# Optimization experiments

Hardware: AMD Instinct MI355X
Metric: run time of the kernel (lower is better)

The kernel has to match this reference:

```python
import jax, jax.numpy as jnp
import numpy as np

NUM_HEADS = 4


def _mha_pool(seg):
    """seg: [n_seg, S, H]. First 4 channels are attention logits (softmax over S),
    rest are values split into 4 heads; returns [n_seg, H-4]."""
    n_seg, S, H = seg.shape
    attn = jax.nn.softmax(seg[:, :, :NUM_HEADS], axis=1)          # [n, S, 4]
    vals = seg[:, :, NUM_HEADS:].reshape(n_seg, S, NUM_HEADS, -1)  # [n, S, 4, hd]
    pooled = jnp.einsum('nsh,nshd->nhd', attn, vals)               # [n, 4, hd]
    return pooled.reshape(n_seg, -1)


def setup_inputs() -> dict:
    key = jax.random.key(0)
    k1, k2, k3, k4 = jax.random.split(key, 4)
    T, D, H = 131072, 2048, 260
    embeddings = jax.random.normal(k1, (T, D), dtype=jnp.float32)
    labels = jax.random.randint(k2, (T,), 0, 2, dtype=jnp.int32)
    W_down = jax.random.normal(k3, (D, H), dtype=jnp.float32) / np.sqrt(D)
    b_down = jnp.zeros((H,), dtype=jnp.float32)
    W_final = jax.random.normal(k4, (H - NUM_HEADS, 1), dtype=jnp.float32) / np.sqrt(H - NUM_HEADS)
    b_final = jnp.zeros((1,), dtype=jnp.float32)
    return {
        'embeddings': embeddings,
        'W_down': W_down,
        'b_down': b_down,
        'W_final': W_final,
        'b_final': b_final,
        'labels': labels,
        'tokens_per_problem': 512,
        'tokens_per_line': 16,
    }


def reference(embeddings, W_down, b_down, W_final, b_final, labels,
              tokens_per_problem, tokens_per_line):
    T, D = embeddings.shape
    H = W_down.shape[1]
    # Dropout is identity in eval mode (reference baseline).
    proj = embeddings @ W_down + b_down                      # [T, H]
    # MHA_POOL_4_HEADS: keep attention logits raw, GELU (exact erf) the values.
    act = jnp.concatenate(
        [proj[:, :NUM_HEADS], jax.nn.gelu(proj[:, NUM_HEADS:], approximate=False)],
        axis=1)                                              # [T, H]

    P = T // tokens_per_problem
    problem_feat = _mha_pool(act.reshape(P, tokens_per_problem, H))   # [P, H-4]
    problem_logits = (problem_feat @ W_final + b_final)[:, 0]

    L = T // tokens_per_line
    line_feat = _mha_pool(act.reshape(L, tokens_per_line, H))         # [L, H-4]
    line_logits = (line_feat @ W_final + b_final)[:, 0]

    token_logits = (act[:, NUM_HEADS:] @ W_final + b_final)[:, 0]     # [T]

    problem_labels = labels.reshape(P, tokens_per_problem).min(axis=1)
    line_labels = labels.reshape(L, tokens_per_line).min(axis=1)
    return token_logits, line_logits, line_labels, problem_logits, problem_labels
```

## Files before the change

### kernel.cpp

```cpp
#include <hip/hip_runtime.h>
#include <hip/hip_bf16.h>
#include <math.h>

#define T_TOK   131072
#define D_IN    2048
#define H_CH    260
#define NFRAG_P 18
#define KSTEPS  64
#define STEP_BYTES  (NFRAG_P * 64 * 16)
#define CHUNK_BYTES (2 * STEP_BYTES)
#define NCHUNK  32

typedef __attribute__((ext_vector_type(8))) short bf16x8;
typedef __attribute__((ext_vector_type(4))) float f32x4;

__device__ inline short f2bf(float x) {
    __hip_bfloat16 h = __float2bfloat16(x);
    return __builtin_bit_cast(short, h);
}

__global__ void prep_wfrag(const float* __restrict__ W, __hip_bfloat16* __restrict__ Wf) {
    int g = blockIdx.x;
    int s = g / NFRAG_P, f = g % NFRAG_P;
    int lane = threadIdx.x;
    int k0 = s * 32 + (lane >> 4) * 8;
    int col = f * 16 + (lane & 15);
    short vals8[8];
#pragma unroll
    for (int j = 0; j < 8; j++) {
        float v = (col < H_CH) ? W[(size_t)(k0 + j) * H_CH + col] : 0.f;
        vals8[j] = f2bf(v);
    }
    *reinterpret_cast<bf16x8*>(reinterpret_cast<short*>(Wf) + ((size_t)g * 64 + lane) * 8) =
        *reinterpret_cast<bf16x8*>(vals8);
}

__global__ __launch_bounds__(512, 4)
void gemm_act(const float* __restrict__ emb, const __hip_bfloat16* __restrict__ Wfrag,
              const float* __restrict__ b_down, const float* __restrict__ W_final,
              const float* __restrict__ b_final,
              float* __restrict__ attnL, __hip_bfloat16* __restrict__ vals,
              float* __restrict__ token_logits) {
    __shared__ __align__(16) char smem[2 * CHUNK_BYTES];
    __shared__ float tokred[8][32];

    int wave = threadIdx.x >> 6;
    int lane = threadIdx.x & 63;
    int quad = wave & 3;
    int nhalf = wave >> 2;
    int f0 = nhalf * 9;
    int r0 = blockIdx.x * 128 + quad * 32;
    int row_in = lane & 15;
    int kbase = (lane >> 4) * 8;

    const char* gW = (const char*)Wfrag;

    auto stage_chunk = [&](int c, char* lbase) {
        const char* src = gW + (size_t)c * CHUNK_BYTES;
#pragma unroll
        for (int r = 0; r < 4; ++r) {
            int off = (r * 8 + wave) * 1024;
            __builtin_amdgcn_global_load_lds(
                (const __attribute__((address_space(1))) unsigned int*)(src + off + lane * 16),
                (__attribute__((address_space(3))) unsigned int*)(lbase + off), 16, 0, 0);
        }
        if (wave < 4) {
            int off = (32 + wave) * 1024;
            __builtin_amdgcn_global_load_lds(
                (const __attribute__((address_space(1))) unsigned int*)(src + off + lane * 16),
                (__attribute__((address_space(3))) unsigned int*)(lbase + off), 16, 0, 0);
        }
    };

    f32x4 acc0[9], acc1[9];
#pragma unroll
    for (int f = 0; f < 9; f++) {
        acc0[f] = (f32x4){0.f, 0.f, 0.f, 0.f};
        acc1[f] = (f32x4){0.f, 0.f, 0.f, 0.f};
    }

    const float* ap0 = emb + (size_t)(r0 + row_in) * D_IN + kbase;
    const float* ap1 = ap0 + (size_t)16 * D_IN;

    stage_chunk(0, smem);
    f32x4 c0l = *reinterpret_cast<const f32x4*>(ap0);
    f32x4 c0h = *reinterpret_cast<const f32x4*>(ap0 + 4);
    f32x4 c1l = *reinterpret_cast<const f32x4*>(ap1);
    f32x4 c1h = *reinterpret_cast<const f32x4*>(ap1 + 4);
    f32x4 n0l, n0h, n1l, n1h;
    __syncthreads();

#define DO_STEP(AL0, AH0, AL1, AH1, BOFF)                                         \
    {                                                                             \
        bf16x8 af0, af1;                                                          \
        af0[0] = f2bf(AL0[0]); af0[1] = f2bf(AL0[1]);                             \
        af0[2] = f2bf(AL0[2]); af0[3] = f2bf(AL0[3]);                             \
        af0[4] = f2bf(AH0[0]); af0[5] = f2bf(AH0[1]);                             \
        af0[6] = f2bf(AH0[2]); af0[7] = f2bf(AH0[3]);                             \
        af1[0] = f2bf(AL1[0]); af1[1] = f2bf(AL1[1]);                             \
        af1[2] = f2bf(AL1[2]); af1[3] = f2bf(AL1[3]);                             \
        af1[4] = f2bf(AH1[0]); af1[5] = f2bf(AH1[1]);                             \
        af1[6] = f2bf(AH1[2]); af1[7] = f2bf(AH1[3]);                             \
        const char* bb = smem + (BOFF) + (size_t)f0 * 1024 + lane * 16;           \
        _Pragma("unroll")                                                         \
        for (int f = 0; f < 9; f++) {                                             \
            bf16x8 bfr = *reinterpret_cast<const bf16x8*>(bb + f * 1024);         \
            acc0[f] = __builtin_amdgcn_mfma_f32_16x16x32_bf16(af0, bfr, acc0[f], 0, 0, 0); \
            acc1[f] = __builtin_amdgcn_mfma_f32_16x16x32_bf16(af1, bfr, acc1[f], 0, 0, 0); \
        }                                                                         \
    }

    for (int c = 0; c < NCHUNK; ++c) {
        int base = (c & 1) * CHUNK_BYTES;
        if (c + 1 < NCHUNK) stage_chunk(c + 1, smem + ((c + 1) & 1) * CHUNK_BYTES);

        int off1 = (2 * c + 1) * 32;
        n0l = *reinterpret_cast<const f32x4*>(ap0 + off1);
        n0h = *reinterpret_cast<const f32x4*>(ap0 + off1 + 4);
        n1l = *reinterpret_cast<const f32x4*>(ap1 + off1);
        n1h = *reinterpret_cast<const f32x4*>(ap1 + off1 + 4);
        DO_STEP(c0l, c0h, c1l, c1h, base)

        int s2 = 2 * c + 2;
        int off2 = (s2 < KSTEPS ? s2 : 0) * 32;
        c0l = *reinterpret_cast<const f32x4*>(ap0 + off2);
        c0h = *reinterpret_cast<const f32x4*>(ap0 + off2 + 4);
        c1l = *reinterpret_cast<const f32x4*>(ap1 + off2);
        c1h = *reinterpret_cast<const f32x4*>(ap1 + off2 + 4);
        DO_STEP(n0l, n0h, n1l, n1h, base + STEP_BYTES)

        __syncthreads();
    }
#undef DO_STEP

    int colbase = lane & 15;
    int rgroup = (lane >> 4) * 4;
    float tp0[4] = {0.f, 0.f, 0.f, 0.f};
    float tp1[4] = {0.f, 0.f, 0.f, 0.f};
#pragma unroll
    for (int f = 0; f < 9; f++) {
        int n = (f0 + f) * 16 + colbase;
        float bias = (n < H_CH) ? b_down[n] : 0.f;
        float wf = (n >= 4 && n < H_CH) ? W_final[n - 4] : 0.f;
#pragma unroll
        for (int i = 0; i < 4; i++) {
            int row0 = r0 + rgroup + i;
            int row1 = row0 + 16;
            float v0 = acc0[f][i] + bias;
            float v1 = acc1[f][i] + bias;
            float a0 = (n < 4) ? v0 : 0.5f * v0 * (1.f + erff(v0 * 0.70710678118f));
            float a1 = (n < 4) ? v1 : 0.5f * v1 * (1.f + erff(v1 * 0.70710678118f));
            if (n < 4) {
                attnL[(size_t)row0 * 4 + n] = v0;
                attnL[(size_t)row1 * 4 + n] = v1;
            } else if (n < H_CH) {
                vals[(size_t)row0 * 256 + (n - 4)] = __float2bfloat16(a0);
                vals[(size_t)row1 * 256 + (n - 4)] = __float2bfloat16(a1);
            }
            tp0[i] += a0 * wf;
            tp1[i] += a1 * wf;
        }
    }
#pragma unroll
    for (int i = 0; i < 4; i++) {
        float v0 = tp0[i], v1 = tp1[i];
        v0 += __shfl_xor(v0, 1); v1 += __shfl_xor(v1, 1);
        v0 += __shfl_xor(v0, 2); v1 += __shfl_xor(v1, 2);
        v0 += __shfl_xor(v0, 4); v1 += __shfl_xor(v1, 4);
        v0 += __shfl_xor(v0, 8); v1 += __shfl_xor(v1, 8);
        if ((lane & 15) == 0) {
            tokred[wave][rgroup + i]      = v0;
            tokred[wave][16 + rgroup + i] = v1;
        }
    }
    __syncthreads();
    if (threadIdx.x < 128) {
        int q = threadIdx.x >> 5, j = threadIdx.x & 31;
        token_logits[blockIdx.x * 128 + q * 32 + j] =
            tokred[q][j] + tokred[4 + q][j] + b_final[0];
    }
}

__global__ __launch_bounds__(256)
void pool_problem(const float* __restrict__ attnL, const __hip_bfloat16* __restrict__ vals,
                  const int* __restrict__ labels,
                  const float* __restrict__ W_final, const float* __restrict__ b_final,
                  float* __restrict__ out_logits, float* __restrict__ out_labels) {
    __shared__ float w_lds[512 * 4];
    __shared__ float wred[4][4];
    __shared__ float psum[4];
    __shared__ int   lred[4];

    int p = blockIdx.x;
    int t = threadIdx.x;
    int lane = t & 63, wid = t >> 6;
    const float* abase = attnL + (size_t)p * 512 * 4;

    f32x4 v0 = *reinterpret_cast<const f32x4*>(abase + (size_t)t * 4);
    f32x4 v1 = *reinterpret_cast<const f32x4*>(abase + (size_t)(t + 256) * 4);

    float mh[4];
#pragma unroll
    for (int h = 0; h < 4; h++) mh[h] = fmaxf(v0[h], v1[h]);
#pragma unroll
    for (int h = 0; h < 4; h++)
        for (int mask = 1; mask < 64; mask <<= 1) mh[h] = fmaxf(mh[h], __shfl_xor(mh[h], mask));
    if (lane == 0) {
#pragma unroll
        for (int h = 0; h < 4; h++) wred[wid][h] = mh[h];
    }
    __syncthreads();
#pragma unroll
    for (int h = 0; h < 4; h++)
        mh[h] = fmaxf(fmaxf(wred[0][h], wred[1][h]), fmaxf(wred[2][h], wred[3][h]));
    __syncthreads();

    float Zh[4];
    f32x4 e0, e1;
#pragma unroll
    for (int h = 0; h < 4; h++) {
        e0[h] = __expf(v0[h] - mh[h]);
        e1[h] = __expf(v1[h] - mh[h]);
        Zh[h] = e0[h] + e1[h];
    }
    *reinterpret_cast<f32x4*>(&w_lds[t * 4]) = e0;
    *reinterpret_cast<f32x4*>(&w_lds[(t + 256) * 4]) = e1;
#pragma unroll
    for (int h = 0; h < 4; h++)
        for (int mask = 1; mask < 64; mask <<= 1) Zh[h] += __shfl_xor(Zh[h], mask);
    if (lane == 0) {
#pragma unroll
        for (int h = 0; h < 4; h++) wred[wid][h] = Zh[h];
    }
    __syncthreads();
#pragma unroll
    for (int h = 0; h < 4; h++) Zh[h] = wred[0][h] + wred[1][h] + wred[2][h] + wred[3][h];

    int h = t >> 6;
    const __hip_bfloat16* col = vals + (size_t)p * 512 * 256 + t;
    float pooled = 0.f;
#pragma unroll 8
    for (int s = 0; s < 512; s++)
        pooled += w_lds[s * 4 + h] * __bfloat162float(col[(size_t)s * 256]);
    float part = (pooled / Zh[h]) * W_final[t];
    for (int mask = 1; mask < 64; mask <<= 1) part += __shfl_xor(part, mask);
    if (lane == 0) psum[wid] = part;

    int lmin = min(labels[p * 512 + t], labels[p * 512 + t + 256]);
    for (int mask = 1; mask < 64; mask <<= 1) lmin = min(lmin, __shfl_xor(lmin, mask));
    if (lane == 0) lred[wid] = lmin;
    __syncthreads();
    if (t == 0) {
        out_logits[p] = psum[0] + psum[1] + psum[2] + psum[3] + b_final[0];
        out_labels[p] = (float)min(min(lred[0], lred[1]), min(lred[2], lred[3]));
    }
}

__global__ __launch_bounds__(256)
void pool_line(const float* __restrict__ attnL, const __hip_bfloat16* __restrict__ vals,
               const int* __restrict__ labels,
               const float* __restrict__ W_final, const float* __restrict__ b_final,
               float* __restrict__ out_logits, float* __restrict__ out_labels) {
    int wid = threadIdx.x >> 6, lane = threadIdx.x & 63;
    int line = blockIdx.x * 4 + wid;

    float x = attnL[(size_t)line * 64 + lane];
    float mm = x;
    mm = fmaxf(mm, __shfl_xor(mm, 4));
    mm = fmaxf(mm, __shfl_xor(mm, 8));
    mm = fmaxf(mm, __shfl_xor(mm, 16));
    mm = fmaxf(mm, __shfl_xor(mm, 32));
    float e = __expf(x - mm);
    float Z = e;
    Z += __shfl_xor(Z, 4);
    Z += __shfl_xor(Z, 8);
    Z += __shfl_xor(Z, 16);
    Z += __shfl_xor(Z, 32);
    float w = e / Z;

    const __hip_bfloat16* vbase = vals + (size_t)line * 16 * 256;
    float logit_part = 0.f;
#pragma unroll
    for (int j = 0; j < 4; j++) {
        float pooled = 0.f;
#pragma unroll
        for (int s = 0; s < 16; s++) {
            float ws = __shfl(w, s * 4 + j);
            pooled += ws * __bfloat162float(vbase[(size_t)s * 256 + j * 64 + lane]);
        }
        logit_part += pooled * W_final[j * 64 + lane];
    }
    for (int mask = 1; mask < 64; mask <<= 1) logit_part += __shfl_xor(logit_part, mask);

    int lab = (lane < 16) ? labels[line * 16 + lane] : 0x7fffffff;
    for (int mask = 1; mask < 64; mask <<= 1) lab = min(lab, __shfl_xor(lab, mask));

    if (lane == 0) {
        out_logits[line] = logit_part + b_final[0];
        out_labels[line] = (float)lab;
    }
}

extern "C" void kernel_launch(void* const* d_in, const int* in_sizes, int n_in,
                              void* d_out, int out_size, void* d_ws, size_t ws_size,
                              hipStream_t stream) {
    const float* emb     = (const float*)d_in[0];
    const float* W_down  = (const float*)d_in[1];
    const float* b_down  = (const float*)d_in[2];
    const float* W_final = (const float*)d_in[3];
    const float* b_final = (const float*)d_in[4];
    const int*   labels  = (const int*)d_in[5];

    float* out      = (float*)d_out;
    float* tok      = out;
    float* line_lg  = out + 131072;
    float* line_lb  = out + 139264;
    float* prob_lg  = out + 147456;
    float* prob_lb  = out + 147712;

    __hip_bfloat16* Wfrag = (__hip_bfloat16*)d_ws;
    float* attnL = (float*)((char*)d_ws + ((size_t)4 << 20));
    __hip_bfloat16* vals = (__hip_bfloat16*)((char*)d_ws + ((size_t)8 << 20));

    prep_wfrag<<<KSTEPS * NFRAG_P, 64, 0, stream>>>(W_down, Wfrag);
    gemm_act<<<T_TOK / 128, 512, 0, stream>>>(emb, Wfrag, b_down, W_final, b_final,
                                              attnL, vals, tok);
    pool_problem<<<256, 256, 0, stream>>>(attnL, vals, labels, W_final, b_final, prob_lg, prob_lb);
    pool_line<<<2048, 256, 0, stream>>>(attnL, vals, labels, W_final, b_final, line_lg, line_lb);
}
```

Baseline: 437.3 us.

## Stage embedding A-tiles through LDS with async global_load_lds double buffering

Embedding rows are now copied from global memory into LDS with async global_load_lds, double-buffered alongside the B fragments one k-step at a time, instead of being read directly into registers by each wave. Because the two waves sharing a row quad both need those rows, this removes the duplicated A loads across the two N-halves and hides their latency behind the MFMA work. In exchange there is one barrier per k-step rather than one per two steps, and each buffer holds fewer bytes.

```diff
diff --git a/kernel.cpp b/kernel.cpp
--- a/kernel.cpp
+++ b/kernel.cpp
@@ -7,9 +7,9 @@
 #define H_CH    260
 #define NFRAG_P 18
 #define KSTEPS  64
-#define STEP_BYTES  (NFRAG_P * 64 * 16)
-#define CHUNK_BYTES (2 * STEP_BYTES)
-#define NCHUNK  32
+#define A_BYTES (8 * 2048)
+#define B_BYTES (NFRAG_P * 64 * 16)
+#define BUF_BYTES (A_BYTES + B_BYTES)
 
 typedef __attribute__((ext_vector_type(8))) short bf16x8;
 typedef __attribute__((ext_vector_type(4))) float f32x4;
@@ -17,6 +17,12 @@
 __device__ inline short f2bf(float x) {
     __hip_bfloat16 h = __float2bfloat16(x);
     return __builtin_bit_cast(short, h);
+}
+
+__device__ inline void glds16(const void* src, void* lds_base_uniform) {
+    __builtin_amdgcn_global_load_lds(
+        (const __attribute__((address_space(1))) unsigned int*)src,
+        (__attribute__((address_space(3))) unsigned int*)lds_base_uniform, 16, 0, 0);
 }
 
 __global__ void prep_wfrag(const float* __restrict__ W, __hip_bfloat16* __restrict__ Wf) {
@@ -41,7 +47,7 @@
               const float* __restrict__ b_final,
               float* __restrict__ attnL, __hip_bfloat16* __restrict__ vals,
               float* __restrict__ token_logits) {
-    __shared__ __align__(16) char smem[2 * CHUNK_BYTES];
+    __shared__ __align__(16) char smem[2 * BUF_BYTES];
     __shared__ float tokred[8][32];
 
     int wave = threadIdx.x >> 6;
@@ -50,26 +56,21 @@
     int nhalf = wave >> 2;
     int f0 = nhalf * 9;
     int r0 = blockIdx.x * 128 + quad * 32;
-    int row_in = lane & 15;
-    int kbase = (lane >> 4) * 8;
 
     const char* gW = (const char*)Wfrag;
-
-    auto stage_chunk = [&](int c, char* lbase) {
-        const char* src = gW + (size_t)c * CHUNK_BYTES;
-#pragma unroll
-        for (int r = 0; r < 4; ++r) {
-            int off = (r * 8 + wave) * 1024;
-            __builtin_amdgcn_global_load_lds(
-                (const __attribute__((address_space(1))) unsigned int*)(src + off + lane * 16),
-                (__attribute__((address_space(3))) unsigned int*)(lbase + off), 16, 0, 0);
-        }
-        if (wave < 4) {
-            int off = (32 + wave) * 1024;
-            __builtin_amdgcn_global_load_lds(
-                (const __attribute__((address_space(1))) unsigned int*)(src + off + lane * 16),
-                (__attribute__((address_space(3))) unsigned int*)(lbase + off), 16, 0, 0);
-        }
+    const float* asrc_base = emb
+        + (size_t)(blockIdx.x * 128 + wave * 16 + (lane & 15)) * D_IN
+        + ((lane >> 4) * 8);
+
+    auto stage_step = [&](int s, char* lbase) {
+        const float* asrc = asrc_base + s * 32;
+        glds16(asrc,     lbase + wave * 2048);
+        glds16(asrc + 4, lbase + wave * 2048 + 1024);
+        const char* bsrc = gW + (size_t)s * B_BYTES + lane * 16;
+        glds16(bsrc + wave * 1024,       lbase + A_BYTES + wave * 1024);
+        glds16(bsrc + (wave + 8) * 1024, lbase + A_BYTES + (wave + 8) * 1024);
+        if (wave < 2)
+            glds16(bsrc + (16 + wave) * 1024, lbase + A_BYTES + (16 + wave) * 1024);
     };
 
     f32x4 acc0[9], acc1[9];
@@ -79,59 +80,33 @@
         acc1[f] = (f32x4){0.f, 0.f, 0.f, 0.f};
     }
 
-    const float* ap0 = emb + (size_t)(r0 + row_in) * D_IN + kbase;
-    const float* ap1 = ap0 + (size_t)16 * D_IN;
-
-    stage_chunk(0, smem);
-    f32x4 c0l = *reinterpret_cast<const f32x4*>(ap0);
-    f32x4 c0h = *reinterpret_cast<const f32x4*>(ap0 + 4);
-    f32x4 c1l = *reinterpret_cast<const f32x4*>(ap1);
-    f32x4 c1h = *reinterpret_cast<const f32x4*>(ap1 + 4);
-    f32x4 n0l, n0h, n1l, n1h;
-    __syncthreads();
-
-#define DO_STEP(AL0, AH0, AL1, AH1, BOFF)                                         \
-    {                                                                             \
-        bf16x8 af0, af1;                                                          \
-        af0[0] = f2bf(AL0[0]); af0[1] = f2bf(AL0[1]);                             \
-        af0[2] = f2bf(AL0[2]); af0[3] = f2bf(AL0[3]);                             \
-        af0[4] = f2bf(AH0[0]); af0[5] = f2bf(AH0[1]);                             \
-        af0[6] = f2bf(AH0[2]); af0[7] = f2bf(AH0[3]);                             \
-        af1[0] = f2bf(AL1[0]); af1[1] = f2bf(AL1[1]);                             \
-        af1[2] = f2bf(AL1[2]); af1[3] = f2bf(AL1[3]);                             \
-        af1[4] = f2bf(AH1[0]); af1[5] = f2bf(AH1[1]);                             \
-        af1[6] = f2bf(AH1[2]); af1[7] = f2bf(AH1[3]);                             \
-        const char* bb = smem + (BOFF) + (size_t)f0 * 1024 + lane * 16;           \
-        _Pragma("unroll")                                                         \
-        for (int f = 0; f < 9; f++) {                                             \
-            bf16x8 bfr = *reinterpret_cast<const bf16x8*>(bb + f * 1024);         \
-            acc0[f] = __builtin_amdgcn_mfma_f32_16x16x32_bf16(af0, bfr, acc0[f], 0, 0, 0); \
-            acc1[f] = __builtin_amdgcn_mfma_f32_16x16x32_bf16(af1, bfr, acc1[f], 0, 0, 0); \
-        }                                                                         \
-    }
-
-    for (int c = 0; c < NCHUNK; ++c) {
-        int base = (c & 1) * CHUNK_BYTES;
-        if (c + 1 < NCHUNK) stage_chunk(c + 1, smem + ((c + 1) & 1) * CHUNK_BYTES);
-
-        int off1 = (2 * c + 1) * 32;
-        n0l = *reinterpret_cast<const f32x4*>(ap0 + off1);
-        n0h = *reinterpret_cast<const f32x4*>(ap0 + off1 + 4);
-        n1l = *reinterpret_cast<const f32x4*>(ap1 + off1);
-        n1h = *reinterpret_cast<const f32x4*>(ap1 + off1 + 4);
-        DO_STEP(c0l, c0h, c1l, c1h, base)
-
-        int s2 = 2 * c + 2;
-        int off2 = (s2 < KSTEPS ? s2 : 0) * 32;
-        c0l = *reinterpret_cast<const f32x4*>(ap0 + off2);
-        c0h = *reinterpret_cast<const f32x4*>(ap0 + off2 + 4);
-        c1l = *reinterpret_cast<const f32x4*>(ap1 + off2);
-        c1h = *reinterpret_cast<const f32x4*>(ap1 + off2 + 4);
-        DO_STEP(n0l, n0h, n1l, n1h, base + STEP_BYTES)
-
+    stage_step(0, smem);
+    __syncthreads();
+
+    for (int s = 0; s < KSTEPS; ++s) {
+        char* cur = smem + (s & 1) * BUF_BYTES;
+        if (s + 1 < KSTEPS) stage_step(s + 1, smem + ((s + 1) & 1) * BUF_BYTES);
+
+        const char* ab = cur + (size_t)(quad * 2) * 2048 + lane * 16;
+        f32x4 a00 = *reinterpret_cast<const f32x4*>(ab);
+        f32x4 a01 = *reinterpret_cast<const f32x4*>(ab + 1024);
+        f32x4 a10 = *reinterpret_cast<const f32x4*>(ab + 2048);
+        f32x4 a11 = *reinterpret_cast<const f32x4*>(ab + 3072);
+        bf16x8 af0, af1;
+        af0[0] = f2bf(a00[0]); af0[1] = f2bf(a00[1]); af0[2] = f2bf(a00[2]); af0[3] = f2bf(a00[3]);
+        af0[4] = f2bf(a01[0]); af0[5] = f2bf(a01[1]); af0[6] = f2bf(a01[2]); af0[7] = f2bf(a01[3]);
+        af1[0] = f2bf(a10[0]); af1[1] = f2bf(a10[1]); af1[2] = f2bf(a10[2]); af1[3] = f2bf(a10[3]);
+        af1[4] = f2bf(a11[0]); af1[5] = f2bf(a11[1]); af1[6] = f2bf(a11[2]); af1[7] = f2bf(a11[3]);
+
+        const char* bb = cur + A_BYTES + (size_t)f0 * 1024 + lane * 16;
+#pragma unroll
+        for (int f = 0; f < 9; f++) {
+            bf16x8 bfr = *reinterpret_cast<const bf16x8*>(bb + f * 1024);
+            acc0[f] = __builtin_amdgcn_mfma_f32_16x16x32_bf16(af0, bfr, acc0[f], 0, 0, 0);
+            acc1[f] = __builtin_amdgcn_mfma_f32_16x16x32_bf16(af1, bfr, acc1[f], 0, 0, 0);
+        }
         __syncthreads();
     }
-#undef DO_STEP
 
     int colbase = lane & 15;
     int rgroup = (lane >> 4) * 4;
```

Measured after the change: 388.9 us. 11.1% less time.
